# Kernel optimization log

Measured on AMD Instinct MI355X. Metric: run time of the kernel, lower is better.

Reference implementation:

```python
import jax, jax.numpy as jnp
import numpy as np

N_NODES = 50000
N_EDGES = 800000
D_IN = 128
D_HID = 128
D_OUT = 128


def setup_inputs() -> dict:
    key = jax.random.key(0)
    ks = jax.random.split(key, 5)
    x = jax.random.normal(ks[0], (N_NODES, D_IN), dtype=jnp.float32)
    edge_index = jax.random.randint(ks[1], (2, N_EDGES), 0, N_NODES, dtype=jnp.int64)
    # Glorot-ish init for the two GCN linear weights (PyG uses glorot)
    W1 = jax.random.normal(ks[2], (D_IN, D_HID), dtype=jnp.float32) * (1.0 / np.sqrt(D_IN))
    b1 = jnp.zeros((D_HID,), dtype=jnp.float32)
    W2 = jax.random.normal(ks[3], (D_HID, D_OUT), dtype=jnp.float32) * (1.0 / np.sqrt(D_HID))
    b2 = jnp.zeros((D_OUT,), dtype=jnp.float32)
    return {"x": x, "edge_index": edge_index, "W1": W1, "b1": b1, "W2": W2, "b2": b2}


def _gcn_layer(x, W, b, src, dst, dinv):
    """PyG GCNConv: h = xW; out[j] = sum_{(i->j)} dinv[i]*dinv[j]*h[i] + dinv[j]^2*h[j] (self-loop) + b."""
    n = x.shape[0]
    h = x @ W                                   # [N, D_out]
    coef = (dinv[src] * dinv[dst])[:, None]     # [E, 1] symmetric norm
    msg = h[src] * coef                         # [E, D_out] gather + scale
    agg = jax.ops.segment_sum(msg, dst, num_segments=n)  # scatter-add
    agg = agg + h * (dinv * dinv)[:, None]      # self-loop contribution
    return agg + b


def reference(x, edge_index, W1, b1, W2, b2):
    src = edge_index[0]
    dst = edge_index[1]
    n = x.shape[0]
    # degree over target nodes, including the added self-loop (+1)
    deg = jax.ops.segment_sum(jnp.ones_like(dst, dtype=x.dtype), dst, num_segments=n) + 1.0
    dinv = jax.lax.rsqrt(deg)
    h = jax.nn.relu(_gcn_layer(x, W1, b1, src, dst, dinv))
    return _gcn_layer(h, W2, b2, src, dst, dinv)
```

## Files before the change

kernel.cpp:

```cpp
#include <hip/hip_runtime.h>
#include <hip/hip_fp16.h>

#define NN 50000
#define NE 800000
#define D 128
#define NBLK ((NN + 255) / 256)

typedef __attribute__((ext_vector_type(8))) short bf16x8;
typedef __attribute__((ext_vector_type(4))) float f32x4;

static __device__ __forceinline__ unsigned short f2bf(float f) {
    unsigned u = __builtin_bit_cast(unsigned, f);
    unsigned r = (u + 0x7fffu + ((u >> 16) & 1u)) >> 16;
    return (unsigned short)r;
}
static __device__ __forceinline__ float bf2f(unsigned short h) {
    unsigned u = ((unsigned)h) << 16;
    return __builtin_bit_cast(float, u);
}

__global__ __launch_bounds__(256) void k_zero_cnt(int* __restrict__ cnt) {
    int i = blockIdx.x * 256 + threadIdx.x;
    if (i < NN) cnt[i] = 0;
}

__global__ __launch_bounds__(256) void k_count(const int* __restrict__ dst, int* __restrict__ cnt,
                                               int* __restrict__ rank) {
    int e = blockIdx.x * 256 + threadIdx.x;
    if (e < NE) rank[e] = atomicAdd(&cnt[dst[e]], 1);
}

__global__ __launch_bounds__(256) void k_scan_partial(const int* __restrict__ cnt, int* __restrict__ blockSums) {
    __shared__ int s[256];
    int t = threadIdx.x;
    int i = blockIdx.x * 256 + t;
    s[t] = (i < NN) ? cnt[i] : 0;
    __syncthreads();
    for (int off = 128; off > 0; off >>= 1) {
        if (t < off) s[t] += s[t + off];
        __syncthreads();
    }
    if (t == 0) blockSums[blockIdx.x] = s[0];
}

__global__ __launch_bounds__(256) void k_scan_blocks(int* __restrict__ blockSums, int* __restrict__ row_ptr) {
    __shared__ int s[256];
    int t = threadIdx.x;
    int v = (t < NBLK) ? blockSums[t] : 0;
    s[t] = v;
    __syncthreads();
    for (int off = 1; off < 256; off <<= 1) {
        int y = (t >= off) ? s[t - off] : 0;
        __syncthreads();
        s[t] += y;
        __syncthreads();
    }
    if (t < NBLK) blockSums[t] = s[t] - v;
    if (t == 0) row_ptr[NN] = NE;
}

__global__ __launch_bounds__(256) void k_scan_final(const int* __restrict__ cnt, const int* __restrict__ blockOffs,
                                                    int* __restrict__ row_ptr, float* __restrict__ dinv) {
    __shared__ int s[256];
    int t = threadIdx.x;
    int i = blockIdx.x * 256 + t;
    int v = (i < NN) ? cnt[i] : 0;
    s[t] = v;
    __syncthreads();
    for (int off = 1; off < 256; off <<= 1) {
        int y = (t >= off) ? s[t - off] : 0;
        __syncthreads();
        s[t] += y;
        __syncthreads();
    }
    if (i < NN) {
        row_ptr[i] = s[t] - v + blockOffs[blockIdx.x];
        dinv[i] = rsqrtf((float)v + 1.0f);
    }
}

__global__ __launch_bounds__(256) void k_fill(const int* __restrict__ src, const int* __restrict__ dst,
                                              const int* __restrict__ rank, const int* __restrict__ row_ptr,
                                              unsigned short* __restrict__ csr) {
    int e = blockIdx.x * 256 + threadIdx.x;
    if (e < NE) {
        int d = dst[e];
        csr[row_ptr[d] + rank[e]] = (unsigned short)src[e];
    }
}

__global__ __launch_bounds__(256) void k_prepw(const float* __restrict__ W1, const float* __restrict__ W2,
                                               char* __restrict__ img1, char* __restrict__ img2) {
    int b = blockIdx.x;
    const float* W = (b < 64) ? W1 : W2;
    char* img = (b < 64) ? img1 : img2;
    int e = (b & 63) * 256 + threadIdx.x;
    int k = e >> 7, n = e & 127;
    float f = W[e];
    unsigned short hi = f2bf(f);
    float rem = f - bf2f(hi);
    unsigned short lo = f2bf(rem);
    unsigned off = (unsigned)((n << 8) + (k << 1)) ^ (unsigned)((n & 7) << 4);
    *(unsigned short*)(img + off) = hi;
    *(unsigned short*)(img + 32768 + off) = lo;
}

template <bool RELU_IN>
__global__ __launch_bounds__(256) void k_mgemm(const float* __restrict__ A, const char* __restrict__ wimg,
                                               __half* __restrict__ H) {
    __shared__ char lds[65536];
    const int t = threadIdx.x;

    {
        const float4* gv = (const float4*)wimg;
        float4* lv = (float4*)lds;
#pragma unroll
        for (int i = 0; i < 16; ++i) lv[i * 256 + t] = gv[i * 256 + t];
    }
    __syncthreads();

    const int lane = t & 63;
    const int wv = t >> 6;
    const int r0 = blockIdx.x * 64 + wv * 16;
    const int rl = lane & 15;
    const int g = lane >> 4;
    int arow = r0 + rl;
    if (arow >= NN) arow = NN - 1;
    const float* ar = A + (size_t)arow * D + g * 8;

    f32x4 acc[8];
#pragma unroll
    for (int j = 0; j < 8; ++j) acc[j] = (f32x4){0.f, 0.f, 0.f, 0.f};

#pragma unroll
    for (int ks = 0; ks < 4; ++ks) {
        float av[8];
        float4 p0 = *(const float4*)(ar + ks * 32);
        float4 p1 = *(const float4*)(ar + ks * 32 + 4);
        av[0] = p0.x; av[1] = p0.y; av[2] = p0.z; av[3] = p0.w;
        av[4] = p1.x; av[5] = p1.y; av[6] = p1.z; av[7] = p1.w;
        bf16x8 ah, al;
#pragma unroll
        for (int i = 0; i < 8; ++i) {
            float a = RELU_IN ? fmaxf(av[i], 0.f) : av[i];
            unsigned short h = f2bf(a);
            ah[i] = (short)h;
            al[i] = (short)f2bf(a - bf2f(h));
        }
        const int kofs = (ks * 32 + g * 8) << 1;
#pragma unroll
        for (int j = 0; j < 8; ++j) {
            int n = j * 16 + rl;
            unsigned off = (unsigned)((n << 8) + kofs) ^ (unsigned)((n & 7) << 4);
            bf16x8 bh = *(const bf16x8*)(lds + off);
            bf16x8 bl = *(const bf16x8*)(lds + 32768 + off);
            acc[j] = __builtin_amdgcn_mfma_f32_16x16x32_bf16(ah, bh, acc[j], 0, 0, 0);
            acc[j] = __builtin_amdgcn_mfma_f32_16x16x32_bf16(ah, bl, acc[j], 0, 0, 0);
            acc[j] = __builtin_amdgcn_mfma_f32_16x16x32_bf16(al, bh, acc[j], 0, 0, 0);
        }
    }

#pragma unroll
    for (int j = 0; j < 8; ++j) {
#pragma unroll
        for (int i = 0; i < 4; ++i) {
            int row = r0 + g * 4 + i;
            if (row < NN) H[(size_t)row * D + j * 16 + rl] = __float2half(acc[j][i]);
        }
    }
}

__global__ __launch_bounds__(256) void k_pull(const __half* __restrict__ H, const float* __restrict__ dinv,
                                              const float* __restrict__ b, const int* __restrict__ row_ptr,
                                              const unsigned short* __restrict__ csr, float* __restrict__ out) {
    int wid = (blockIdx.x * 256 + threadIdx.x) >> 6;
    int lane = threadIdx.x & 63;
    int node = __builtin_amdgcn_readfirstlane(wid);
    int rl = lane & 15;
    int g = lane >> 4;

    float dd = dinv[node];

    float2 a0 = {0.f, 0.f}, a1 = {0.f, 0.f}, a2 = {0.f, 0.f}, a3 = {0.f, 0.f};
    float2 c0b = {0.f, 0.f}, c1b = {0.f, 0.f}, c2b = {0.f, 0.f}, c3b = {0.f, 0.f};

    int beg = row_ptr[node];
    int end = row_ptr[node + 1];
    for (int i = beg + g; i < end; i += 8) {
        int i1 = i + 4;
        bool ok = i1 < end;
        int s0 = csr[i];
        int s1 = csr[ok ? i1 : i];
        float c0 = dinv[s0] * dd;
        float c1 = ok ? dinv[s1] * dd : 0.f;
        float4 raw0 = *(const float4*)(H + (size_t)s0 * D + rl * 8);
        float4 raw1 = *(const float4*)(H + (size_t)s1 * D + rl * 8);
        const __half2* h0 = (const __half2*)&raw0;
        const __half2* h1 = (const __half2*)&raw1;
        float2 f0 = __half22float2(h0[0]);
        float2 f1 = __half22float2(h0[1]);
        float2 f2 = __half22float2(h0[2]);
        float2 f3 = __half22float2(h0[3]);
        a0.x = fmaf(f0.x, c0, a0.x); a0.y = fmaf(f0.y, c0, a0.y);
        a1.x = fmaf(f1.x, c0, a1.x); a1.y = fmaf(f1.y, c0, a1.y);
        a2.x = fmaf(f2.x, c0, a2.x); a2.y = fmaf(f2.y, c0, a2.y);
        a3.x = fmaf(f3.x, c0, a3.x); a3.y = fmaf(f3.y, c0, a3.y);
        float2 g0 = __half22float2(h1[0]);
        float2 g1 = __half22float2(h1[1]);
        float2 g2 = __half22float2(h1[2]);
        float2 g3 = __half22float2(h1[3]);
        c0b.x = fmaf(g0.x, c1, c0b.x); c0b.y = fmaf(g0.y, c1, c0b.y);
        c1b.x = fmaf(g1.x, c1, c1b.x); c1b.y = fmaf(g1.y, c1, c1b.y);
        c2b.x = fmaf(g2.x, c1, c2b.x); c2b.y = fmaf(g2.y, c1, c2b.y);
        c3b.x = fmaf(g3.x, c1, c3b.x); c3b.y = fmaf(g3.y, c1, c3b.y);
    }
    a0.x += c0b.x; a0.y += c0b.y;
    a1.x += c1b.x; a1.y += c1b.y;
    a2.x += c2b.x; a2.y += c2b.y;
    a3.x += c3b.x; a3.y += c3b.y;

    float v[8] = {a0.x, a0.y, a1.x, a1.y, a2.x, a2.y, a3.x, a3.y};
#pragma unroll
    for (int i = 0; i < 8; ++i) {
        v[i] += __shfl_xor(v[i], 16);
        v[i] += __shfl_xor(v[i], 32);
    }

    if (g == 0) {
        float s2 = dd * dd;
        float4 raw = *(const float4*)(H + (size_t)node * D + rl * 8);
        const __half2* hh = (const __half2*)&raw;
        float2 s0 = __half22float2(hh[0]);
        float2 s1 = __half22float2(hh[1]);
        float2 s2v = __half22float2(hh[2]);
        float2 s3 = __half22float2(hh[3]);
        float4 b0 = ((const float4*)b)[rl * 2];
        float4 b1 = ((const float4*)b)[rl * 2 + 1];
        float4 r0, r1;
        r0.x = fmaf(s0.x, s2, v[0] + b0.x);
        r0.y = fmaf(s0.y, s2, v[1] + b0.y);
        r0.z = fmaf(s1.x, s2, v[2] + b0.z);
        r0.w = fmaf(s1.y, s2, v[3] + b0.w);
        r1.x = fmaf(s2v.x, s2, v[4] + b1.x);
        r1.y = fmaf(s2v.y, s2, v[5] + b1.y);
        r1.z = fmaf(s3.x, s2, v[6] + b1.z);
        r1.w = fmaf(s3.y, s2, v[7] + b1.w);
        float4* op = (float4*)(out + (size_t)node * D + rl * 8);
        op[0] = r0;
        op[1] = r1;
    }
}

extern "C" void kernel_launch(void* const* d_in, const int* in_sizes, int n_in,
                              void* d_out, int out_size, void* d_ws, size_t ws_size,
                              hipStream_t stream) {
    const float* x  = (const float*)d_in[0];
    const int*   ei = (const int*)d_in[1];
    const float* W1 = (const float*)d_in[2];
    const float* b1 = (const float*)d_in[3];
    const float* W2 = (const float*)d_in[4];
    const float* b2 = (const float*)d_in[5];
    float* out = (float*)d_out;

    const int* src = ei;
    const int* dst = ei + NE;

    char* ws = (char*)d_ws;
    int*    cnt       = (int*)   (ws + 0);
    int*    row_ptr   = (int*)   (ws + 204800);
    int*    blockSums = (int*)   (ws + 409600);
    float*  dinv      = (float*) (ws + 410624);
    char*   wimg1     = (char*)  (ws + 614400);
    char*   wimg2     = (char*)  (ws + 679936);
    int*    rank      = (int*)   (ws + 745472);
    unsigned short* csr = (unsigned short*)(ws + 3945472);
    __half* h         = (__half*)(ws + 5545472);

    const int nBlkEdge = (NE + 255) / 256;
    const int nBlkGemm = (NN + 63) / 64;
    const int nBlkPull = NN / 4;

    k_zero_cnt<<<NBLK, 256, 0, stream>>>(cnt);
    k_count<<<nBlkEdge, 256, 0, stream>>>(dst, cnt, rank);
    k_scan_partial<<<NBLK, 256, 0, stream>>>(cnt, blockSums);
    k_scan_blocks<<<1, 256, 0, stream>>>(blockSums, row_ptr);
    k_scan_final<<<NBLK, 256, 0, stream>>>(cnt, blockSums, row_ptr, dinv);
    k_fill<<<nBlkEdge, 256, 0, stream>>>(src, dst, rank, row_ptr, csr);
    k_prepw<<<128, 256, 0, stream>>>(W1, W2, wimg1, wimg2);

    k_mgemm<false><<<nBlkGemm, 256, 0, stream>>>(x, wimg1, h);
    k_pull<<<nBlkPull, 256, 0, stream>>>(h, dinv, b1, row_ptr, csr, out);

    k_mgemm<true><<<nBlkGemm, 256, 0, stream>>>(out, wimg2, h);
    k_pull<<<nBlkPull, 256, 0, stream>>>(h, dinv, b2, row_ptr, csr, out);
}
```

Measured before the change: 238.3 us.

## Switch GEMM to fp16 two-term MFMA and store hidden layer as fp16

Replaces the bf16 three-MFMA split-precision GEMM with fp16 inputs, a hi/lo fp16 split of the weights only, and two MFMAs per tile. The first aggregation now writes the hidden activations as fp16 into a separate buffer, so the second GEMM reads half the bytes and applies ReLU with a sign-bit mask. The zero-count kernel is replaced with hipMemsetAsync. The intent is less MFMA work and less memory traffic, at the cost of fp16 rounding on activations and the risk of overflow or lost precision.

```diff
diff --git a/kernel.cpp b/kernel.cpp
--- a/kernel.cpp
+++ b/kernel.cpp
@@ -6,23 +6,9 @@
 #define D 128
 #define NBLK ((NN + 255) / 256)
 
-typedef __attribute__((ext_vector_type(8))) short bf16x8;
+typedef __attribute__((ext_vector_type(8))) _Float16 f16x8;
+typedef __attribute__((ext_vector_type(8))) short short8;
 typedef __attribute__((ext_vector_type(4))) float f32x4;
-
-static __device__ __forceinline__ unsigned short f2bf(float f) {
-    unsigned u = __builtin_bit_cast(unsigned, f);
-    unsigned r = (u + 0x7fffu + ((u >> 16) & 1u)) >> 16;
-    return (unsigned short)r;
-}
-static __device__ __forceinline__ float bf2f(unsigned short h) {
-    unsigned u = ((unsigned)h) << 16;
-    return __builtin_bit_cast(float, u);
-}
-
-__global__ __launch_bounds__(256) void k_zero_cnt(int* __restrict__ cnt) {
-    int i = blockIdx.x * 256 + threadIdx.x;
-    if (i < NN) cnt[i] = 0;
-}
 
 __global__ __launch_bounds__(256) void k_count(const int* __restrict__ dst, int* __restrict__ cnt,
                                                int* __restrict__ rank) {
@@ -97,16 +83,16 @@
     int e = (b & 63) * 256 + threadIdx.x;
     int k = e >> 7, n = e & 127;
     float f = W[e];
-    unsigned short hi = f2bf(f);
-    float rem = f - bf2f(hi);
-    unsigned short lo = f2bf(rem);
+    __half hi = __float2half_rn(f);
+    float rem = f - __half2float(hi);
+    __half lo = __float2half_rn(rem);
     unsigned off = (unsigned)((n << 8) + (k << 1)) ^ (unsigned)((n & 7) << 4);
-    *(unsigned short*)(img + off) = hi;
-    *(unsigned short*)(img + 32768 + off) = lo;
-}
-
-template <bool RELU_IN>
-__global__ __launch_bounds__(256) void k_mgemm(const float* __restrict__ A, const char* __restrict__ wimg,
+    *(__half*)(img + off) = hi;
+    *(__half*)(img + 32768 + off) = lo;
+}
+
+template <bool RELU_IN, bool A_FP16>
+__global__ __launch_bounds__(256) void k_mgemm(const void* __restrict__ Av, const char* __restrict__ wimg,
                                                __half* __restrict__ H) {
     __shared__ char lds[65536];
     const int t = threadIdx.x;
@@ -126,7 +112,6 @@
     const int g = lane >> 4;
     int arow = r0 + rl;
     if (arow >= NN) arow = NN - 1;
-    const float* ar = A + (size_t)arow * D + g * 8;
 
     f32x4 acc[8];
 #pragma unroll
@@ -134,29 +119,39 @@
 
 #pragma unroll
     for (int ks = 0; ks < 4; ++ks) {
-        float av[8];
-        float4 p0 = *(const float4*)(ar + ks * 32);
-        float4 p1 = *(const float4*)(ar + ks * 32 + 4);
-        av[0] = p0.x; av[1] = p0.y; av[2] = p0.z; av[3] = p0.w;
-        av[4] = p1.x; av[5] = p1.y; av[6] = p1.z; av[7] = p1.w;
-        bf16x8 ah, al;
-#pragma unroll
-        for (int i = 0; i < 8; ++i) {
-            float a = RELU_IN ? fmaxf(av[i], 0.f) : av[i];
-            unsigned short h = f2bf(a);
-            ah[i] = (short)h;
-            al[i] = (short)f2bf(a - bf2f(h));
+        f16x8 a;
+        if (A_FP16) {
+            const __half* A = (const __half*)Av;
+            float4 raw = *(const float4*)(A + (size_t)arow * D + ks * 32 + g * 8);
+            if (RELU_IN) {
+                short8 s = __builtin_bit_cast(short8, raw);
+#pragma unroll
+                for (int i = 0; i < 8; ++i) s[i] = (s[i] & (short)0x8000) ? (short)0 : s[i];
+                a = __builtin_bit_cast(f16x8, s);
+            } else {
+                a = __builtin_bit_cast(f16x8, raw);
+            }
+        } else {
+            const float* A = (const float*)Av;
+            const float* ar = A + (size_t)arow * D + ks * 32 + g * 8;
+            float4 p0 = *(const float4*)ar;
+            float4 p1 = *(const float4*)(ar + 4);
+            float av8[8] = {p0.x, p0.y, p0.z, p0.w, p1.x, p1.y, p1.z, p1.w};
+#pragma unroll
+            for (int i = 0; i < 8; ++i) {
+                float f = RELU_IN ? fmaxf(av8[i], 0.f) : av8[i];
+                a[i] = (_Float16)f;
+            }
         }
         const int kofs = (ks * 32 + g * 8) << 1;
 #pragma unroll
         for (int j = 0; j < 8; ++j) {
             int n = j * 16 + rl;
             unsigned off = (unsigned)((n << 8) + kofs) ^ (unsigned)((n & 7) << 4);
-            bf16x8 bh = *(const bf16x8*)(lds + off);
-            bf16x8 bl = *(const bf16x8*)(lds + 32768 + off);
-            acc[j] = __builtin_amdgcn_mfma_f32_16x16x32_bf16(ah, bh, acc[j], 0, 0, 0);
-            acc[j] = __builtin_amdgcn_mfma_f32_16x16x32_bf16(ah, bl, acc[j], 0, 0, 0);
-            acc[j] = __builtin_amdgcn_mfma_f32_16x16x32_bf16(al, bh, acc[j], 0, 0, 0);
+            f16x8 bh = *(const f16x8*)(lds + off);
+            f16x8 bl = *(const f16x8*)(lds + 32768 + off);
+            acc[j] = __builtin_amdgcn_mfma_f32_16x16x32_f16(a, bh, acc[j], 0, 0, 0);
+            acc[j] = __builtin_amdgcn_mfma_f32_16x16x32_f16(a, bl, acc[j], 0, 0, 0);
         }
     }
 
@@ -170,9 +165,10 @@
     }
 }
 
+template <bool OUT_FP16>
 __global__ __launch_bounds__(256) void k_pull(const __half* __restrict__ H, const float* __restrict__ dinv,
                                               const float* __restrict__ b, const int* __restrict__ row_ptr,
-                                              const unsigned short* __restrict__ csr, float* __restrict__ out) {
+                                              const unsigned short* __restrict__ csr, void* __restrict__ outv) {
     int wid = (blockIdx.x * 256 + threadIdx.x) >> 6;
     int lane = threadIdx.x & 63;
     int node = __builtin_amdgcn_readfirstlane(wid);
@@ -235,19 +231,30 @@
         float2 s2v = __half22float2(hh[2]);
         float2 s3 = __half22float2(hh[3]);
         float4 b0 = ((const float4*)b)[rl * 2];
-        float4 b1 = ((const float4*)b)[rl * 2 + 1];
-        float4 r0, r1;
-        r0.x = fmaf(s0.x, s2, v[0] + b0.x);
-        r0.y = fmaf(s0.y, s2, v[1] + b0.y);
-        r0.z = fmaf(s1.x, s2, v[2] + b0.z);
-        r0.w = fmaf(s1.y, s2, v[3] + b0.w);
-        r1.x = fmaf(s2v.x, s2, v[4] + b1.x);
-        r1.y = fmaf(s2v.y, s2, v[5] + b1.y);
-        r1.z = fmaf(s3.x, s2, v[6] + b1.z);
-        r1.w = fmaf(s3.y, s2, v[7] + b1.w);
-        float4* op = (float4*)(out + (size_t)node * D + rl * 8);
-        op[0] = r0;
-        op[1] = r1;
+        float4 b1v = ((const float4*)b)[rl * 2 + 1];
+        float r[8];
+        r[0] = fmaf(s0.x, s2, v[0] + b0.x);
+        r[1] = fmaf(s0.y, s2, v[1] + b0.y);
+        r[2] = fmaf(s1.x, s2, v[2] + b0.z);
+        r[3] = fmaf(s1.y, s2, v[3] + b0.w);
+        r[4] = fmaf(s2v.x, s2, v[4] + b1v.x);
+        r[5] = fmaf(s2v.y, s2, v[5] + b1v.y);
+        r[6] = fmaf(s3.x, s2, v[6] + b1v.z);
+        r[7] = fmaf(s3.y, s2, v[7] + b1v.w);
+        if (OUT_FP16) {
+            __half* out = (__half*)outv;
+            __half2 o[4];
+            o[0] = __floats2half2_rn(r[0], r[1]);
+            o[1] = __floats2half2_rn(r[2], r[3]);
+            o[2] = __floats2half2_rn(r[4], r[5]);
+            o[3] = __floats2half2_rn(r[6], r[7]);
+            *(float4*)(out + (size_t)node * D + rl * 8) = *(float4*)o;
+        } else {
+            float* out = (float*)outv;
+            float* op = out + (size_t)node * D + rl * 8;
+            *(float4*)op = make_float4(r[0], r[1], r[2], r[3]);
+            *(float4*)(op + 4) = make_float4(r[4], r[5], r[6], r[7]);
+        }
     }
 }
 
@@ -275,12 +282,13 @@
     int*    rank      = (int*)   (ws + 745472);
     unsigned short* csr = (unsigned short*)(ws + 3945472);
     __half* h         = (__half*)(ws + 5545472);
+    __half* h2        = (__half*)(ws + 18345472);
 
     const int nBlkEdge = (NE + 255) / 256;
     const int nBlkGemm = (NN + 63) / 64;
     const int nBlkPull = NN / 4;
 
-    k_zero_cnt<<<NBLK, 256, 0, stream>>>(cnt);
+    hipMemsetAsync(cnt, 0, (size_t)NN * 4, stream);
     k_count<<<nBlkEdge, 256, 0, stream>>>(dst, cnt, rank);
     k_scan_partial<<<NBLK, 256, 0, stream>>>(cnt, blockSums);
     k_scan_blocks<<<1, 256, 0, stream>>>(blockSums, row_ptr);
@@ -288,9 +296,9 @@
     k_fill<<<nBlkEdge, 256, 0, stream>>>(src, dst, rank, row_ptr, csr);
     k_prepw<<<128, 256, 0, stream>>>(W1, W2, wimg1, wimg2);
 
-    k_mgemm<false><<<nBlkGemm, 256, 0, stream>>>(x, wimg1, h);
-    k_pull<<<nBlkPull, 256, 0, stream>>>(h, dinv, b1, row_ptr, csr, out);
-
-    k_mgemm<true><<<nBlkGemm, 256, 0, stream>>>(out, wimg2, h);
-    k_pull<<<nBlkPull, 256, 0, stream>>>(h, dinv, b2, row_ptr, csr, out);
-}
+    k_mgemm<false, false><<<nBlkGemm, 256, 0, stream>>>(x, wimg1, h);
+    k_pull<true><<<nBlkPull, 256, 0, stream>>>(h, dinv, b1, row_ptr, csr, h2);
+
+    k_mgemm<true, true><<<nBlkGemm, 256, 0, stream>>>(h2, wimg2, h);
+    k_pull<false><<<nBlkPull, 256, 0, stream>>>(h, dinv, b2, row_ptr, csr, out);
+}
```

Result: no change. 234.1 us (-1.7%).
